# Kernel optimization log

Measured on AMD Instinct MI355X. Metric: run time of the kernel, lower is better.

Reference implementation:

```python
import jax, jax.numpy as jnp
import numpy as np

B, S, HID = 2, 2048, 2048
NH, NKV, HD = 16, 4, 128
GROUPS = NH // NKV
CLIP = 8.0
ROPE_THETA = 500000.0
QKV_OUT = HID + 2 * NKV * HD  # 3072
NEG = jnp.finfo(jnp.float32).min


def setup_inputs() -> dict:
    key = jax.random.key(0)
    k1, k2, k3 = jax.random.split(key, 3)
    hidden_states = jax.random.normal(k1, (B, S, HID), dtype=jnp.float32)
    position_ids = jnp.tile(jnp.arange(S, dtype=jnp.int64)[None, :], (B, 1))
    Wqkv = jax.random.normal(k2, (QKV_OUT, HID), dtype=jnp.float32) * (HID ** -0.5)
    Wout = jax.random.normal(k3, (HID, HID), dtype=jnp.float32) * (HID ** -0.5)
    return {"hidden_states": hidden_states, "position_ids": position_ids,
            "Wqkv": Wqkv, "Wout": Wout}


def _rotate_half(x):
    x1, x2 = jnp.split(x, 2, axis=-1)
    return jnp.concatenate((-x2, x1), axis=-1)


def reference(hidden_states, position_ids, Wqkv, Wout):
    b, s, _ = hidden_states.shape
    # fused QKV projection + clamp
    qkv = jnp.einsum('bsh,oh->bso', hidden_states, Wqkv)
    qkv = jnp.clip(qkv, -CLIP, CLIP)
    q, k, v = jnp.split(qkv, [HID, HID + NKV * HD], axis=2)
    q = q.reshape(b, s, NH, HD).transpose(0, 2, 1, 3)   # [b, nh, s, hd]
    k = k.reshape(b, s, NKV, HD).transpose(0, 2, 1, 3)  # [b, nkv, s, hd]
    v = v.reshape(b, s, NKV, HD).transpose(0, 2, 1, 3)
    # rotary embedding
    inv_freq = 1.0 / (ROPE_THETA ** (jnp.arange(0, HD, 2, dtype=jnp.float32) / HD))
    freqs = position_ids.astype(jnp.float32)[:, :, None] * inv_freq[None, None, :]  # [b,s,hd/2]
    emb = jnp.concatenate((freqs, freqs), axis=-1)      # [b, s, hd]
    cos = jnp.cos(emb)[:, None, :, :]                   # [b, 1, s, hd]
    sin = jnp.sin(emb)[:, None, :, :]
    q = q * cos + _rotate_half(q) * sin
    k = k * cos + _rotate_half(k) * sin
    # repeat kv heads (GQA)
    k = jnp.repeat(k, GROUPS, axis=1)  # [b, nh, s, hd]
    v = jnp.repeat(v, GROUPS, axis=1)
    # attention with additive causal mask
    scores = jnp.einsum('bhqd,bhkd->bhqk', q, k) / jnp.sqrt(jnp.float32(HD))
    causal = jnp.where(jnp.tril(jnp.ones((s, s), dtype=bool)), 0.0, NEG)
    scores = scores + causal[None, None, :, :]
    attn = jax.nn.softmax(scores.astype(jnp.float32), axis=-1).astype(q.dtype)
    out = jnp.einsum('bhqk,bhkd->bhqd', attn, v)
    out = out.transpose(0, 2, 1, 3).reshape(b, s, HID)
    return jnp.einsum('bsh,oh->bso', out, Wout)
```

## Files before the change

### kernel.cpp

```cpp
#include <hip/hip_runtime.h>
#include <stdint.h>

#define S_    2048
#define HID_  2048
#define NH_   16
#define NKV_  4
#define HD_   128

using short4x = __attribute__((ext_vector_type(4))) short;
using short8  = __attribute__((ext_vector_type(8))) short;
using floatx4 = __attribute__((ext_vector_type(4))) float;

#define NEGBIG (-3.0e38f)

__device__ __forceinline__ unsigned short f2bf(float x) {
  union { float f; unsigned u; } v; v.f = x;
  unsigned r = v.u + 0x7fffu + ((v.u >> 16) & 1u);
  return (unsigned short)(r >> 16);
}
__device__ __forceinline__ float bf2f(unsigned short b) {
  union { unsigned u; float f; } v; v.u = ((unsigned)b) << 16;
  return v.f;
}
__device__ __forceinline__ void ld_lds16(const void* g, void* l) {
  __builtin_amdgcn_global_load_lds(
      (const __attribute__((address_space(1))) unsigned*)g,
      (__attribute__((address_space(3))) unsigned*)l, 16, 0, 0);
}

__global__ void k_cvt3(const float* __restrict__ s0, unsigned short* __restrict__ d0, int n0,
                       const float* __restrict__ s1, unsigned short* __restrict__ d1, int n1,
                       const float* __restrict__ s2, unsigned short* __restrict__ d2, int n2) {
  int i = blockIdx.x * blockDim.x + threadIdx.x;
  const float* s; unsigned short* d;
  if (i < n0) { s = s0; d = d0; }
  else if (i < n0 + n1) { s = s1; d = d1; i -= n0; }
  else { s = s2; d = d2; i -= n0 + n1; if (i >= n2) return; }
  float4 v = ((const float4*)s)[i];
  union { unsigned short us[4]; uint2 u2; } u;
  u.us[0] = f2bf(v.x); u.us[1] = f2bf(v.y); u.us[2] = f2bf(v.z); u.us[3] = f2bf(v.w);
  ((uint2*)d)[i] = u.u2;
}

__global__ void k_rope2(unsigned short* __restrict__ Qb, unsigned short* __restrict__ Kb,
                        const int* __restrict__ pos, int nQ, float qscale) {
  int idx = blockIdx.x * blockDim.x + threadIdx.x;
  unsigned short* buf; int nh; float oscale;
  if (idx < nQ) { buf = Qb; nh = NH_; oscale = qscale; }
  else { buf = Kb; nh = NKV_; oscale = 1.0f; idx -= nQ; }
  int d = idx & 63;
  int h = (idx >> 6) % nh;
  int m = idx / (unsigned)(nh << 6);
  float p = (float)pos[m];
  float inv = expf(-(float)d * (13.122363377404328f / 64.0f));
  float f = p * inv;
  float cs = cosf(f), sn = sinf(f);
  size_t base = (size_t)m * (nh * HD_) + h * HD_ + d;
  float x1 = bf2f(buf[base]), x2 = bf2f(buf[base + 64]);
  buf[base]      = f2bf((x1 * cs - x2 * sn) * oscale);
  buf[base + 64] = f2bf((x2 * cs + x1 * sn) * oscale);
}

template <int EPI>
__global__ void __launch_bounds__(256)
k_gemm_bt(const unsigned short* __restrict__ A, const unsigned short* __restrict__ Bw,
          unsigned short* __restrict__ Qb, unsigned short* __restrict__ Kb,
          unsigned short* __restrict__ Vt, float* __restrict__ Of) {
  const int K = HID_;
  __shared__ __align__(16) unsigned short As[2][128 * 32];
  __shared__ __align__(16) unsigned short Bs[2][128 * 32];
  const int tid  = threadIdx.x;
  const int wave = tid >> 6, lane = tid & 63;
  const int quad = lane >> 4, l15 = lane & 15;
  const int wm = (wave >> 1) * 64, wn = (wave & 1) * 64;
  const int m0 = blockIdx.x * 128, n0 = blockIdx.y * 128;

  floatx4 acc[4][4] = {};

  const int srow = tid >> 2;
  const int scol = (tid & 3) * 8;
  const unsigned short* Ag0 = A  + (size_t)(m0 + srow)      * K + scol;
  const unsigned short* Ag1 = A  + (size_t)(m0 + 64 + srow) * K + scol;
  const unsigned short* Bg0 = Bw + (size_t)(n0 + srow)      * K + scol;
  const unsigned short* Bg1 = Bw + (size_t)(n0 + 64 + srow) * K + scol;

  auto stage = [&](int buf, int k0) {
    ld_lds16(Ag0 + k0, &As[buf][tid * 8]);
    ld_lds16(Ag1 + k0, &As[buf][2048 + tid * 8]);
    ld_lds16(Bg0 + k0, &Bs[buf][tid * 8]);
    ld_lds16(Bg1 + k0, &Bs[buf][2048 + tid * 8]);
  };

  stage(0, 0);
  int cur = 0;
  for (int k0 = 0; k0 < K; k0 += 32) {
    __syncthreads();
    if (k0 + 32 < K) stage(cur ^ 1, k0 + 32);
    short8 a[4], b[4];
#pragma unroll
    for (int i = 0; i < 4; i++) a[i] = *(const short8*)&As[cur][(wm + i * 16 + l15) * 32 + quad * 8];
#pragma unroll
    for (int j = 0; j < 4; j++) b[j] = *(const short8*)&Bs[cur][(wn + j * 16 + l15) * 32 + quad * 8];
#pragma unroll
    for (int i = 0; i < 4; i++)
#pragma unroll
      for (int j = 0; j < 4; j++)
        acc[i][j] = __builtin_amdgcn_mfma_f32_16x16x32_bf16(a[i], b[j], acc[i][j], 0, 0, 0);
    cur ^= 1;
  }

#pragma unroll
  for (int i = 0; i < 4; i++) {
#pragma unroll
    for (int j = 0; j < 4; j++) {
      const int col = n0 + wn + j * 16 + l15;
#pragma unroll
      for (int r = 0; r < 4; r++) {
        const int row = m0 + wm + i * 16 + quad * 4 + r;
        float x = acc[i][j][r];
        if (EPI == 0) {
          x = fminf(fmaxf(x, -8.0f), 8.0f);
          if (col < HID_) {
            Qb[(size_t)row * HID_ + col] = f2bf(x);
          } else if (col < HID_ + NKV_ * HD_) {
            Kb[(size_t)row * (NKV_ * HD_) + (col - HID_)] = f2bf(x);
          } else {
            int oo = col - (HID_ + NKV_ * HD_);
            int kvh = oo >> 7, d = oo & 127;
            int bb = row >> 11, ss = row & 2047;
            Vt[((size_t)((bb * NKV_ + kvh) * HD_ + d) << 11) + ss] = f2bf(x);
          }
        } else {
          Of[(size_t)row * HID_ + col] = x;
        }
      }
    }
  }
}

__global__ void __launch_bounds__(256, 2)
k_attn(const unsigned short* __restrict__ Qb, const unsigned short* __restrict__ Kb,
       const unsigned short* __restrict__ Vt, unsigned short* __restrict__ AO) {
  __shared__ __align__(16) unsigned short sm[2][16384];
  __shared__ __align__(16) unsigned short Pl[4][16][80];

  const int tid  = threadIdx.x;
  const int wave = tid >> 6, lane = tid & 63;
  const int quad = lane >> 4, l15 = lane & 15;
  const int tLow  = blockIdx.x;
  const int tHigh = 31 - tLow;
  const int q0L = tLow * 64, q0H = tHigh * 64;
  const int bh = blockIdx.y;
  const int b = bh >> 4, h = bh & 15;
  const int kvh = h >> 2;

  const int srow = tid >> 2;
  const int scol = (tid & 3) * 8;

  {
    const unsigned short* qgL = Qb + (size_t)(b * S_ + q0L + srow) * HID_ + h * HD_ + scol;
    const unsigned short* qgH = Qb + (size_t)(b * S_ + q0H + srow) * HID_ + h * HD_ + scol;
#pragma unroll
    for (int i = 0; i < 4; i++) ld_lds16(qgL + i * 32, &sm[0][i * 2048 + tid * 8]);
#pragma unroll
    for (int i = 0; i < 4; i++) ld_lds16(qgH + i * 32, &sm[1][i * 2048 + tid * 8]);
  }
  __syncthreads();
  short8 qaL[4], qaH[4];
#pragma unroll
  for (int c = 0; c < 4; c++) {
    qaL[c] = *(const short8*)&sm[0][(c * 64 + wave * 16 + l15) * 32 + quad * 8];
    qaH[c] = *(const short8*)&sm[1][(c * 64 + wave * 16 + l15) * 32 + quad * 8];
  }
  __syncthreads();

  floatx4 oacL[8] = {}, oacH[8] = {};
  floatx4 oacEL = {}, oacEH = {};
  float mL = NEGBIG, mH = NEGBIG;

  const unsigned short* kgb = Kb + (size_t)b * S_ * (NKV_ * HD_) + kvh * HD_ + scol;
  const unsigned short* vgb = Vt + (size_t)(b * NKV_ + kvh) * HD_ * S_;

  unsigned short* PlW = &Pl[wave][0][0];

  short8 ones;
#pragma unroll
  for (int i = 0; i < 8; i++) ones[i] = (short)0x3F80;

  auto stage = [&](int bufI, int j) {
    unsigned short* B = &sm[bufI][0];
    const unsigned short* kg = kgb + (size_t)(j * 64 + srow) * (NKV_ * HD_);
#pragma unroll
    for (int i = 0; i < 4; i++) ld_lds16(kg + i * 32, &B[i * 2048 + tid * 8]);
#pragma unroll
    for (int i = 0; i < 4; i++) {
      int c = i >> 1, rowd = (i & 1) * 64 + srow;
      ld_lds16(vgb + (size_t)rowd * S_ + j * 64 + c * 32 + scol,
               &B[8192 + c * 4096 + (i & 1) * 2048 + tid * 8]);
    }
  };

  auto attn_step = [&](const short8* qa, floatx4* oac, floatx4& oacE, float& m_run,
                       int q0, int j, bool diag, const unsigned short* Kt,
                       const unsigned short* Vts) {
    floatx4 sc[4] = {};
#pragma unroll
    for (int t = 0; t < 4; t++)
#pragma unroll
      for (int c = 0; c < 4; c++) {
        short8 ka = *(const short8*)&Kt[c * 2048 + (t * 16 + l15) * 32 + quad * 8];
        sc[t] = __builtin_amdgcn_mfma_f32_16x16x32_bf16(ka, qa[c], sc[t], 0, 0, 0);
      }

    if (diag) {
      const int rowq = q0 + wave * 16 + l15;
#pragma unroll
      for (int t = 0; t < 4; t++) {
        const int kb0 = j * 64 + t * 16 + quad * 4;
#pragma unroll
        for (int r = 0; r < 4; r++)
          if (kb0 + r > rowq) sc[t][r] = NEGBIG;
      }
    }

    float mx = sc[0][0];
#pragma unroll
    for (int t = 0; t < 4; t++)
#pragma unroll
      for (int r = 0; r < 4; r++) mx = fmaxf(mx, sc[t][r]);
    mx = fmaxf(mx, __shfl_xor(mx, 16));
    mx = fmaxf(mx, __shfl_xor(mx, 32));

    const float mo = m_run;
    m_run = fmaxf(mo, mx);
    if (__any(mx > mo)) {
      float alpha = __builtin_amdgcn_exp2f(mo - m_run);
      float al4[4];
#pragma unroll
      for (int r = 0; r < 4; r++) al4[r] = __shfl(alpha, quad * 4 + r, 16);
#pragma unroll
      for (int t = 0; t < 8; t++)
#pragma unroll
        for (int r = 0; r < 4; r++) oac[t][r] *= al4[r];
#pragma unroll
      for (int r = 0; r < 4; r++) oacE[r] *= al4[r];
    }

#pragma unroll
    for (int t = 0; t < 4; t++) {
      short4x pk;
#pragma unroll
      for (int r = 0; r < 4; r++)
        pk[r] = (short)f2bf(__builtin_amdgcn_exp2f(sc[t][r] - m_run));
      *(short4x*)&PlW[l15 * 80 + t * 16 + quad * 4] = pk;
    }

    short8 pa0 = *(const short8*)&PlW[l15 * 80 + quad * 8];
    short8 pa1 = *(const short8*)&PlW[l15 * 80 + 32 + quad * 8];
#pragma unroll
    for (int t = 0; t < 8; t++) {
      short8 vb0 = *(const short8*)&Vts[(t * 16 + l15) * 32 + quad * 8];
      oac[t] = __builtin_amdgcn_mfma_f32_16x16x32_bf16(pa0, vb0, oac[t], 0, 0, 0);
      short8 vb1 = *(const short8*)&Vts[4096 + (t * 16 + l15) * 32 + quad * 8];
      oac[t] = __builtin_amdgcn_mfma_f32_16x16x32_bf16(pa1, vb1, oac[t], 0, 0, 0);
    }
    oacE = __builtin_amdgcn_mfma_f32_16x16x32_bf16(pa0, ones, oacE, 0, 0, 0);
    oacE = __builtin_amdgcn_mfma_f32_16x16x32_bf16(pa1, ones, oacE, 0, 0, 0);
  };

  stage(0, 0);
  int cur = 0;
  for (int j = 0; j <= tHigh; ++j) {
    __syncthreads();
    if (j < tHigh) stage(cur ^ 1, j + 1);
    const unsigned short* Kt  = &sm[cur][0];
    const unsigned short* Vts = Kt + 8192;
    attn_step(qaH, oacH, oacEH, mH, q0H, j, j == tHigh, Kt, Vts);
    if (j <= tLow) attn_step(qaL, oacL, oacEL, mL, q0L, j, j == tLow, Kt, Vts);
    cur ^= 1;
  }

#pragma unroll
  for (int t = 0; t < 8; t++)
#pragma unroll
    for (int r = 0; r < 4; r++) {
      int rgL = q0L + wave * 16 + quad * 4 + r;
      int rgH = q0H + wave * 16 + quad * 4 + r;
      AO[(size_t)(b * S_ + rgL) * HID_ + h * HD_ + t * 16 + l15] = f2bf(oacL[t][r] / oacEL[r]);
      AO[(size_t)(b * S_ + rgH) * HID_ + h * HD_ + t * 16 + l15] = f2bf(oacH[t][r] / oacEH[r]);
    }
}

extern "C" void kernel_launch(void* const* d_in, const int* in_sizes, int n_in,
                              void* d_out, int out_size, void* d_ws, size_t ws_size,
                              hipStream_t stream) {
  (void)in_sizes; (void)n_in; (void)out_size; (void)ws_size;
  const float* hidden = (const float*)d_in[0];
  const int*   pos    = (const int*)d_in[1];
  const float* Wqkv   = (const float*)d_in[2];
  const float* Wout   = (const float*)d_in[3];
  float* out = (float*)d_out;

  unsigned short* ws = (unsigned short*)d_ws;
  const size_t M1 = 1024 * 1024;
  unsigned short* hb  = ws;
  unsigned short* wqb = ws + 8 * M1;
  unsigned short* wob = ws + 14 * M1;
  unsigned short* Qb  = ws + 18 * M1;
  unsigned short* Kb  = ws + 26 * M1;
  unsigned short* Vt  = ws + 28 * M1;
  unsigned short* AO  = hb;

  const float QSCL = 0.08838834764831845f * 1.4426950408889634f;
  const int nQrope = 2 * 2048 * NH_ * 64;
  const int nKrope = 2 * 2048 * NKV_ * 64;

  k_cvt3<<<18432, 256, 0, stream>>>(hidden, hb, 2097152,
                                    Wqkv, wqb, 1572864,
                                    Wout, wob, 1048576);
  k_gemm_bt<0><<<dim3(32, 24), 256, 0, stream>>>(hb, wqb, Qb, Kb, Vt, nullptr);
  k_rope2<<<(nQrope + nKrope) / 256, 256, 0, stream>>>(Qb, Kb, pos, nQrope, QSCL);
  k_attn<<<dim3(16, 32), 256, 0, stream>>>(Qb, Kb, Vt, AO);
  k_gemm_bt<1><<<dim3(32, 16), 256, 0, stream>>>(AO, wob, nullptr, nullptr, nullptr, out);
}
```

Baseline: 329.3 us.

## Share K/V fragment loads across paired query tiles; single-buffer GEMM LDS

In the attention kernel, the high and low query tiles are now processed together whenever both are active. Each K and V LDS fragment is loaded once and feeds two MFMAs, which halves LDS reads and interleaves independent MFMA chains. Separately, the projection GEMM drops LDS double-buffering in favour of a single buffer with two barriers per k-step. That cuts LDS use and may raise occupancy, but it gives up the overlap of global loads with MFMA work. Holding both score sets at once raises register pressure.

```diff
diff --git a/kernel.cpp b/kernel.cpp
--- a/kernel.cpp
+++ b/kernel.cpp
@@ -67,8 +67,8 @@
           unsigned short* __restrict__ Qb, unsigned short* __restrict__ Kb,
           unsigned short* __restrict__ Vt, float* __restrict__ Of) {
   const int K = HID_;
-  __shared__ __align__(16) unsigned short As[2][128 * 32];
-  __shared__ __align__(16) unsigned short Bs[2][128 * 32];
+  __shared__ __align__(16) unsigned short As[128 * 32];
+  __shared__ __align__(16) unsigned short Bs[128 * 32];
   const int tid  = threadIdx.x;
   const int wave = tid >> 6, lane = tid & 63;
   const int quad = lane >> 4, l15 = lane & 15;
@@ -83,30 +83,28 @@
   const unsigned short* Ag1 = A  + (size_t)(m0 + 64 + srow) * K + scol;
   const unsigned short* Bg0 = Bw + (size_t)(n0 + srow)      * K + scol;
   const unsigned short* Bg1 = Bw + (size_t)(n0 + 64 + srow) * K + scol;
-
-  auto stage = [&](int buf, int k0) {
-    ld_lds16(Ag0 + k0, &As[buf][tid * 8]);
-    ld_lds16(Ag1 + k0, &As[buf][2048 + tid * 8]);
-    ld_lds16(Bg0 + k0, &Bs[buf][tid * 8]);
-    ld_lds16(Bg1 + k0, &Bs[buf][2048 + tid * 8]);
-  };
-
-  stage(0, 0);
-  int cur = 0;
+  unsigned short* lA0 = &As[tid * 8];
+  unsigned short* lA1 = &As[2048 + tid * 8];
+  unsigned short* lB0 = &Bs[tid * 8];
+  unsigned short* lB1 = &Bs[2048 + tid * 8];
+
   for (int k0 = 0; k0 < K; k0 += 32) {
     __syncthreads();
-    if (k0 + 32 < K) stage(cur ^ 1, k0 + 32);
+    ld_lds16(Ag0 + k0, lA0);
+    ld_lds16(Ag1 + k0, lA1);
+    ld_lds16(Bg0 + k0, lB0);
+    ld_lds16(Bg1 + k0, lB1);
+    __syncthreads();
     short8 a[4], b[4];
 #pragma unroll
-    for (int i = 0; i < 4; i++) a[i] = *(const short8*)&As[cur][(wm + i * 16 + l15) * 32 + quad * 8];
-#pragma unroll
-    for (int j = 0; j < 4; j++) b[j] = *(const short8*)&Bs[cur][(wn + j * 16 + l15) * 32 + quad * 8];
+    for (int i = 0; i < 4; i++) a[i] = *(const short8*)&As[(wm + i * 16 + l15) * 32 + quad * 8];
+#pragma unroll
+    for (int j = 0; j < 4; j++) b[j] = *(const short8*)&Bs[(wn + j * 16 + l15) * 32 + quad * 8];
 #pragma unroll
     for (int i = 0; i < 4; i++)
 #pragma unroll
       for (int j = 0; j < 4; j++)
         acc[i][j] = __builtin_amdgcn_mfma_f32_16x16x32_bf16(a[i], b[j], acc[i][j], 0, 0, 0);
-    cur ^= 1;
   }
 
 #pragma unroll
@@ -200,18 +198,8 @@
     }
   };
 
-  auto attn_step = [&](const short8* qa, floatx4* oac, floatx4& oacE, float& m_run,
-                       int q0, int j, bool diag, const unsigned short* Kt,
-                       const unsigned short* Vts) {
-    floatx4 sc[4] = {};
-#pragma unroll
-    for (int t = 0; t < 4; t++)
-#pragma unroll
-      for (int c = 0; c < 4; c++) {
-        short8 ka = *(const short8*)&Kt[c * 2048 + (t * 16 + l15) * 32 + quad * 8];
-        sc[t] = __builtin_amdgcn_mfma_f32_16x16x32_bf16(ka, qa[c], sc[t], 0, 0, 0);
-      }
-
+  auto softmax_tile = [&](floatx4* sc, floatx4* oac, floatx4& oacE, float& m_run,
+                          int q0, int j, bool diag, short8& pa0, short8& pa1) {
     if (diag) {
       const int rowq = q0 + wave * 16 + l15;
 #pragma unroll
@@ -222,7 +210,6 @@
           if (kb0 + r > rowq) sc[t][r] = NEGBIG;
       }
     }
-
     float mx = sc[0][0];
 #pragma unroll
     for (int t = 0; t < 4; t++)
@@ -245,7 +232,6 @@
 #pragma unroll
       for (int r = 0; r < 4; r++) oacE[r] *= al4[r];
     }
-
 #pragma unroll
     for (int t = 0; t < 4; t++) {
       short4x pk;
@@ -254,18 +240,59 @@
         pk[r] = (short)f2bf(__builtin_amdgcn_exp2f(sc[t][r] - m_run));
       *(short4x*)&PlW[l15 * 80 + t * 16 + quad * 4] = pk;
     }
-
-    short8 pa0 = *(const short8*)&PlW[l15 * 80 + quad * 8];
-    short8 pa1 = *(const short8*)&PlW[l15 * 80 + 32 + quad * 8];
+    pa0 = *(const short8*)&PlW[l15 * 80 + quad * 8];
+    pa1 = *(const short8*)&PlW[l15 * 80 + 32 + quad * 8];
+  };
+
+  auto step_two = [&](int j, const unsigned short* Kt, const unsigned short* Vts,
+                      bool diagL, bool diagH) {
+    floatx4 scH[4] = {}, scL[4] = {};
+#pragma unroll
+    for (int t = 0; t < 4; t++)
+#pragma unroll
+      for (int c = 0; c < 4; c++) {
+        short8 ka = *(const short8*)&Kt[c * 2048 + (t * 16 + l15) * 32 + quad * 8];
+        scH[t] = __builtin_amdgcn_mfma_f32_16x16x32_bf16(ka, qaH[c], scH[t], 0, 0, 0);
+        scL[t] = __builtin_amdgcn_mfma_f32_16x16x32_bf16(ka, qaL[c], scL[t], 0, 0, 0);
+      }
+    short8 paH0, paH1, paL0, paL1;
+    softmax_tile(scH, oacH, oacEH, mH, q0H, j, diagH, paH0, paH1);
+    softmax_tile(scL, oacL, oacEL, mL, q0L, j, diagL, paL0, paL1);
 #pragma unroll
     for (int t = 0; t < 8; t++) {
       short8 vb0 = *(const short8*)&Vts[(t * 16 + l15) * 32 + quad * 8];
-      oac[t] = __builtin_amdgcn_mfma_f32_16x16x32_bf16(pa0, vb0, oac[t], 0, 0, 0);
+      oacH[t] = __builtin_amdgcn_mfma_f32_16x16x32_bf16(paH0, vb0, oacH[t], 0, 0, 0);
+      oacL[t] = __builtin_amdgcn_mfma_f32_16x16x32_bf16(paL0, vb0, oacL[t], 0, 0, 0);
       short8 vb1 = *(const short8*)&Vts[4096 + (t * 16 + l15) * 32 + quad * 8];
-      oac[t] = __builtin_amdgcn_mfma_f32_16x16x32_bf16(pa1, vb1, oac[t], 0, 0, 0);
-    }
-    oacE = __builtin_amdgcn_mfma_f32_16x16x32_bf16(pa0, ones, oacE, 0, 0, 0);
-    oacE = __builtin_amdgcn_mfma_f32_16x16x32_bf16(pa1, ones, oacE, 0, 0, 0);
+      oacH[t] = __builtin_amdgcn_mfma_f32_16x16x32_bf16(paH1, vb1, oacH[t], 0, 0, 0);
+      oacL[t] = __builtin_amdgcn_mfma_f32_16x16x32_bf16(paL1, vb1, oacL[t], 0, 0, 0);
+    }
+    oacEH = __builtin_amdgcn_mfma_f32_16x16x32_bf16(paH0, ones, oacEH, 0, 0, 0);
+    oacEH = __builtin_amdgcn_mfma_f32_16x16x32_bf16(paH1, ones, oacEH, 0, 0, 0);
+    oacEL = __builtin_amdgcn_mfma_f32_16x16x32_bf16(paL0, ones, oacEL, 0, 0, 0);
+    oacEL = __builtin_amdgcn_mfma_f32_16x16x32_bf16(paL1, ones, oacEL, 0, 0, 0);
+  };
+
+  auto step_one = [&](int j, const unsigned short* Kt, const unsigned short* Vts, bool diagH) {
+    floatx4 scH[4] = {};
+#pragma unroll
+    for (int t = 0; t < 4; t++)
+#pragma unroll
+      for (int c = 0; c < 4; c++) {
+        short8 ka = *(const short8*)&Kt[c * 2048 + (t * 16 + l15) * 32 + quad * 8];
+        scH[t] = __builtin_amdgcn_mfma_f32_16x16x32_bf16(ka, qaH[c], scH[t], 0, 0, 0);
+      }
+    short8 paH0, paH1;
+    softmax_tile(scH, oacH, oacEH, mH, q0H, j, diagH, paH0, paH1);
+#pragma unroll
+    for (int t = 0; t < 8; t++) {
+      short8 vb0 = *(const short8*)&Vts[(t * 16 + l15) * 32 + quad * 8];
+      oacH[t] = __builtin_amdgcn_mfma_f32_16x16x32_bf16(paH0, vb0, oacH[t], 0, 0, 0);
+      short8 vb1 = *(const short8*)&Vts[4096 + (t * 16 + l15) * 32 + quad * 8];
+      oacH[t] = __builtin_amdgcn_mfma_f32_16x16x32_bf16(paH1, vb1, oacH[t], 0, 0, 0);
+    }
+    oacEH = __builtin_amdgcn_mfma_f32_16x16x32_bf16(paH0, ones, oacEH, 0, 0, 0);
+    oacEH = __builtin_amdgcn_mfma_f32_16x16x32_bf16(paH1, ones, oacEH, 0, 0, 0);
   };
 
   stage(0, 0);
@@ -275,8 +302,8 @@
     if (j < tHigh) stage(cur ^ 1, j + 1);
     const unsigned short* Kt  = &sm[cur][0];
     const unsigned short* Vts = Kt + 8192;
-    attn_step(qaH, oacH, oacEH, mH, q0H, j, j == tHigh, Kt, Vts);
-    if (j <= tLow) attn_step(qaL, oacL, oacEL, mL, q0L, j, j == tLow, Kt, Vts);
+    if (j <= tLow) step_two(j, Kt, Vts, j == tLow, j == tHigh);
+    else           step_one(j, Kt, Vts, j == tHigh);
     cur ^= 1;
   }
 
```

Measured after the change: 319.6 us. 1.03x faster.
